# Kernel tuning notes

Hardware: AMD Instinct MI355X
Metric: run time of the kernel (lower is better)

The kernel has to match this reference:

```python
import jax, jax.numpy as jnp
import numpy as np

N_E = 1024
E_DIM = 256
BETA = 0.25
EPS = 1e-10


def setup_inputs() -> dict:
    key = jax.random.key(0)
    k1, k2 = jax.random.split(key)
    z = jax.random.normal(k1, (32, E_DIM, 32, 32), dtype=jnp.float32)
    emb = jax.random.normal(k2, (N_E, E_DIM), dtype=jnp.float32)
    return {"z": z, "emb": emb}


def reference(z, emb):
    sg = jax.lax.stop_gradient
    # (B, C, H, W) -> (B, H, W, C)
    zp = jnp.transpose(z, (0, 2, 3, 1))
    zf = zp.reshape(-1, E_DIM)  # (N, C), N = B*H*W
    # squared euclidean distances: ||z||^2 + ||e||^2 - 2 z e^T  -> (N, n_e)
    d = (jnp.sum(zf * zf, axis=1, keepdims=True)
         + jnp.sum(emb * emb, axis=1)
         - 2.0 * jnp.matmul(zf, emb.T))
    idx = jnp.argmin(d, axis=1)  # (N,)
    # one-hot @ codebook == gather (same math, no dense one-hot matmul)
    z_q1 = emb[idx].reshape(zp.shape)  # (B, H, W, C)
    # loss: note original does NOT detach z_q1 anywhere
    loss = jnp.mean((z_q1 - zp) ** 2) + BETA * jnp.mean((z_q1 - sg(zp)) ** 2)
    # straight-through (original detaches z, not z_q1)
    z_q = zp + (z_q1 - sg(zp))
    # perplexity from mean one-hot encodings = normalized histogram of indices
    counts = jnp.bincount(idx, length=N_E)
    e_mean = counts.astype(zf.dtype) / idx.shape[0]
    perplexity = jnp.exp(-jnp.sum(e_mean * jnp.log(e_mean + EPS)))
    z_q = jnp.transpose(z_q, (0, 3, 1, 2))
    z_q1_out = jnp.transpose(z_q1, (0, 3, 1, 2))
    return loss, z_q, perplexity, idx, z_q1_out
```

## Files before the change

### kernel.cpp

```cpp
#include <hip/hip_runtime.h>
#include <hip/hip_bf16.h>
#include <math.h>

#define CDIM 256
#define HW   1024
#define NVEC 32768
#define NE   1024
#define ZSIZE 8388608
#define NSPLIT 2
#define MARGIN 0.05f

#define OUT_LOSS 0
#define OUT_ZQ   1
#define OUT_PERP 8388609
#define OUT_IDX  8388610
#define OUT_ZQ1  8421378

#define WS_LOSS   0
#define WS_RCNT   64
#define WS_HIST   128
#define WS_ENORM  4224
#define WS_IDX    8448
#define WS_RLIST  139520
#define WS_S1     270592
#define WS_S2     532736
#define WS_J1     794880
#define WS_EBH    1057024
#define WS_EBL    1581312
#define WS_ZBH    2105600
#define WS_ZBL    18882816
#define WS_SCORE  WS_EBH

typedef __attribute__((ext_vector_type(8))) short short8;
typedef __attribute__((ext_vector_type(4))) float f32x4;
typedef __attribute__((ext_vector_type(8))) unsigned short ushort8v;

__device__ __forceinline__ unsigned short bf16_rne(float x) {
    union { float f; unsigned u; } v; v.f = x;
    unsigned r = v.u + 0x7FFFu + ((v.u >> 16) & 1u);
    return (unsigned short)(r >> 16);
}
__device__ __forceinline__ float bf16_to_f(unsigned short h) {
    union { unsigned u; float f; } v; v.u = ((unsigned)h) << 16;
    return v.f;
}
__device__ __forceinline__ void lds_barrier() {
    asm volatile("s_waitcnt lgkmcnt(0)\n\ts_barrier" ::: "memory");
}

__global__ __launch_bounds__(256) void vq_prep(
    const float* __restrict__ z, const float* __restrict__ emb,
    unsigned short* __restrict__ zbh, unsigned short* __restrict__ zbl,
    unsigned short* __restrict__ ebh, unsigned short* __restrict__ ebl,
    float* __restrict__ enorm)
{
    const int tid = threadIdx.x, w = tid >> 6, L = tid & 63;
    if (blockIdx.x < 512) {
        __shared__ unsigned short th[64 * 264];
        __shared__ unsigned short tl[64 * 264];
        const int b = blockIdx.x >> 4, hw0 = (blockIdx.x & 15) << 6;
        const float* zp = z + (size_t)b * (CDIM * HW) + hw0;
        for (int i = 0; i < 16; ++i) {
            int k = (i * 4 + w) * 4;
            float f0 = zp[(size_t)(k + 0) * HW + L];
            float f1 = zp[(size_t)(k + 1) * HW + L];
            float f2 = zp[(size_t)(k + 2) * HW + L];
            float f3 = zp[(size_t)(k + 3) * HW + L];
            ushort4 hi = { bf16_rne(f0), bf16_rne(f1), bf16_rne(f2), bf16_rne(f3) };
            ushort4 lo = { bf16_rne(f0 - bf16_to_f(hi.x)), bf16_rne(f1 - bf16_to_f(hi.y)),
                           bf16_rne(f2 - bf16_to_f(hi.z)), bf16_rne(f3 - bf16_to_f(hi.w)) };
            *(ushort4*)&th[L * 264 + k] = hi;
            *(ushort4*)&tl[L * 264 + k] = lo;
        }
        __syncthreads();
#pragma unroll
        for (int it = 0; it < 8; ++it) {
            int row = it * 8 + (tid >> 5);
            int kc = (tid & 31) * 8;
            size_t o = (size_t)(b * 1024 + hw0 + row) * CDIM + kc;
            *(ushort8v*)(zbh + o) = *(ushort8v*)&th[row * 264 + kc];
            *(ushort8v*)(zbl + o) = *(ushort8v*)&tl[row * 264 + kc];
        }
    } else {
        const int cb = (int)(blockIdx.x - 512) * 64;
        for (int p = 0; p < 16; ++p) {
            int code = cb + p * 4 + w;
            float4 v = *(const float4*)(emb + (size_t)code * CDIM + L * 4);
            float s = v.x * v.x + v.y * v.y + v.z * v.z + v.w * v.w;
            for (int off = 32; off; off >>= 1) s += __shfl_down(s, off, 64);
            if (L == 0) enorm[code] = s;
            ushort4 hi = { bf16_rne(v.x), bf16_rne(v.y), bf16_rne(v.z), bf16_rne(v.w) };
            ushort4 lo = { bf16_rne(v.x - bf16_to_f(hi.x)), bf16_rne(v.y - bf16_to_f(hi.y)),
                           bf16_rne(v.z - bf16_to_f(hi.z)), bf16_rne(v.w - bf16_to_f(hi.w)) };
            *(ushort4*)(ebh + (size_t)code * CDIM + L * 4) = hi;
            *(ushort4*)(ebl + (size_t)code * CDIM + L * 4) = lo;
        }
    }
}

__global__ __launch_bounds__(256, 2) void vq_mfma3(
    const unsigned short* __restrict__ zbh, const unsigned short* __restrict__ zbl,
    const unsigned short* __restrict__ ebh, const unsigned short* __restrict__ ebl,
    const float* __restrict__ enorm,
    float* __restrict__ s1_ws, float* __restrict__ s2_ws, int* __restrict__ j1_ws)
{
    __shared__ short albuf[32768];
    __shared__ short bbuf[8192];

    const int tid = threadIdx.x, w = tid >> 6, L = tid & 63;
    const int l15 = L & 15, q = L >> 4;
    const int r16 = tid & 15, ch = (tid >> 4) & 3;
    const int mtile = blockIdx.x & 255, js = blockIdx.x >> 8;
    const int n0 = mtile << 7;
    const int jsbase = js << 9;

#pragma unroll
    for (int ro = 0; ro < 16; ++ro) {
        const int seg = ro * 4 + w;
        const int sw2 = seg >> 4, smf = (seg >> 3) & 1, skk = seg & 7;
        short8 v = *(const short8*)(zbl + (size_t)(n0 + sw2 * 32 + smf * 16 + r16) * CDIM + skk * 32 + ch * 8);
        *(short8*)(albuf + seg * 512 + L * 8) = v;
    }
    short8 AH[2][8];
#pragma unroll
    for (int mf = 0; mf < 2; ++mf)
#pragma unroll
        for (int kk = 0; kk < 8; ++kk)
            AH[mf][kk] = *(const short8*)(zbh + (size_t)(n0 + w * 32 + mf * 16 + l15) * CDIM + kk * 32 + q * 8);
    __syncthreads();

    float s1[2][4], s2[2][4]; int j1[2][4];
#pragma unroll
    for (int mf = 0; mf < 2; ++mf)
#pragma unroll
        for (int r = 0; r < 4; ++r) { s1[mf][r] = -3.4e38f; s2[mf][r] = -3.4e38f; j1[mf][r] = 0; }

    for (int j0i = 0; j0i < 4; ++j0i) {
        const int j0 = jsbase + j0i * 128;
        f32x4 acc[2][8] = {};
        short8 st[4];
#pragma unroll
        for (int ro = 0; ro < 4; ++ro) {
            const unsigned short* src = (ro >= 2) ? ebl : ebh;
            const int jf = (ro & 1) * 4 + w;
            st[ro] = *(const short8*)(src + (size_t)(j0 + jf * 16 + r16) * CDIM + ch * 8);
        }
#pragma unroll
        for (int kk = 0; kk < 8; ++kk) {
            lds_barrier();
#pragma unroll
            for (int ro = 0; ro < 4; ++ro)
                *(short8*)(bbuf + (ro * 4 + w) * 512 + L * 8) = st[ro];
            if (kk < 7) {
                const int k0n = (kk + 1) * 32;
#pragma unroll
                for (int ro = 0; ro < 4; ++ro) {
                    const unsigned short* src = (ro >= 2) ? ebl : ebh;
                    const int jf = (ro & 1) * 4 + w;
                    st[ro] = *(const short8*)(src + (size_t)(j0 + jf * 16 + r16) * CDIM + k0n + ch * 8);
                }
            }
            lds_barrier();
            short8 AL0 = *(const short8*)(albuf + (w * 16 + kk) * 512 + L * 8);
            short8 AL1 = *(const short8*)(albuf + (w * 16 + 8 + kk) * 512 + L * 8);
#pragma unroll
            for (int jf = 0; jf < 8; ++jf) {
                short8 Bh = *(const short8*)(bbuf + jf * 512 + L * 8);
                short8 Bl = *(const short8*)(bbuf + (8 + jf) * 512 + L * 8);
                acc[0][jf] = __builtin_amdgcn_mfma_f32_16x16x32_bf16(AH[0][kk], Bh, acc[0][jf], 0, 0, 0);
                acc[1][jf] = __builtin_amdgcn_mfma_f32_16x16x32_bf16(AH[1][kk], Bh, acc[1][jf], 0, 0, 0);
                acc[0][jf] = __builtin_amdgcn_mfma_f32_16x16x32_bf16(AH[0][kk], Bl, acc[0][jf], 0, 0, 0);
                acc[1][jf] = __builtin_amdgcn_mfma_f32_16x16x32_bf16(AH[1][kk], Bl, acc[1][jf], 0, 0, 0);
                acc[0][jf] = __builtin_amdgcn_mfma_f32_16x16x32_bf16(AL0, Bh, acc[0][jf], 0, 0, 0);
                acc[1][jf] = __builtin_amdgcn_mfma_f32_16x16x32_bf16(AL1, Bh, acc[1][jf], 0, 0, 0);
            }
        }
#pragma unroll
        for (int jf = 0; jf < 8; ++jf) {
            const int j = j0 + jf * 16 + l15;
            const float hn = 0.5f * enorm[j];
#pragma unroll
            for (int mf = 0; mf < 2; ++mf)
#pragma unroll
                for (int r = 0; r < 4; ++r) {
                    float s = acc[mf][jf][r] - hn;
                    if (s > s1[mf][r]) { s2[mf][r] = s1[mf][r]; s1[mf][r] = s; j1[mf][r] = j; }
                    else if (s > s2[mf][r]) s2[mf][r] = s;
                }
        }
    }

#pragma unroll
    for (int mf = 0; mf < 2; ++mf)
#pragma unroll
        for (int r = 0; r < 4; ++r) {
            float a1 = s1[mf][r], a2 = s2[mf][r]; int aj = j1[mf][r];
            for (int m = 1; m < 16; m <<= 1) {
                float o1 = __shfl_xor(a1, m, 64);
                float o2 = __shfl_xor(a2, m, 64);
                int   oj = __shfl_xor(aj, m, 64);
                if (o1 > a1 || (o1 == a1 && oj < aj)) { a2 = fmaxf(a1, o2); a1 = o1; aj = oj; }
                else a2 = fmaxf(a2, o1);
            }
            if (l15 == 0) {
                int o = js * NVEC + n0 + w * 32 + mf * 16 + q * 4 + r;
                s1_ws[o] = a1; s2_ws[o] = a2; j1_ws[o] = aj;
            }
        }
}

__global__ __launch_bounds__(256) void vq_merge(
    const float* __restrict__ s1_ws, const float* __restrict__ s2_ws,
    const int* __restrict__ j1_ws, int* __restrict__ idx_ws,
    float* __restrict__ idx_out, int* __restrict__ hist,
    int* __restrict__ rcnt, int* __restrict__ rlist,
    unsigned long long* __restrict__ score)
{
    int n = blockIdx.x * 256 + threadIdx.x;
    score[n] = 0ull;
    float b1 = -3.4e38f, b2 = -3.4e38f; int bj = 0;
#pragma unroll
    for (int s = 0; s < NSPLIT; ++s) {
        float a1 = s1_ws[s * NVEC + n], a2 = s2_ws[s * NVEC + n];
        int aj = j1_ws[s * NVEC + n];
        if (a1 > b1 || (a1 == b1 && aj < bj)) { b2 = fmaxf(b1, a2); b1 = a1; bj = aj; }
        else b2 = fmaxf(b2, a1);
    }
    idx_ws[n] = bj;
    if (b1 - b2 < MARGIN) {
        int p = atomicAdd(rcnt, 1); rlist[p] = n;
    } else {
        idx_out[n] = (float)bj;
        atomicAdd(&hist[bj], 1);
    }
}

__global__ __launch_bounds__(256) void vq_rescue(
    const float* __restrict__ z, const float* __restrict__ emb,
    const float* __restrict__ enorm, const int* __restrict__ rcnt,
    const int* __restrict__ rlist, unsigned long long* __restrict__ score)
{
    __shared__ __align__(16) float zrow[256];
    __shared__ float en_s[64];
    __shared__ float rs[4];
    __shared__ int   rj[4];
    const int tid = threadIdx.x;
    const int wv = tid >> 6, L = tid & 63;
    const int chunk = blockIdx.x & 15;
    const int jwave = chunk * 64 + wv * 16;
    const int jodd = L >> 5;
    const int rstride = gridDim.x >> 4;
    const int count = *rcnt;

    for (int it = blockIdx.x >> 4; it < count; it += rstride) {
        __syncthreads();
        const int n = rlist[it];
        zrow[tid] = z[(size_t)(n >> 10) * (CDIM * HW) + (size_t)tid * HW + (n & 1023)];
        if (tid < 64) en_s[tid] = enorm[chunk * 64 + tid];
        __syncthreads();
        const float4 zv = *(const float4*)&zrow[L * 4];

        float b1 = -3.4e38f; int bj = 0x7fffffff;
#pragma unroll
        for (int jo = 0; jo < 16; jo += 2) {
            const int jA = jwave + jo;
            const float4 eA = *(const float4*)(emb + (size_t)jA * CDIM + L * 4);
            const float4 eB = *(const float4*)(emb + (size_t)(jA + 1) * CDIM + L * 4);
            float pA = fmaf(zv.x, eA.x, fmaf(zv.y, eA.y, fmaf(zv.z, eA.z, zv.w * eA.w)));
            float pB = fmaf(zv.x, eB.x, fmaf(zv.y, eB.y, fmaf(zv.z, eB.z, zv.w * eB.w)));
            float tA = pA + __shfl_xor(pA, 32, 64);
            float tB = pB + __shfl_xor(pB, 32, 64);
            float u = (L < 32) ? tA : tB;
            u += __shfl_xor(u, 16, 64);
            u += __shfl_xor(u, 8, 64);
            u += __shfl_xor(u, 4, 64);
            u += __shfl_xor(u, 2, 64);
            u += __shfl_xor(u, 1, 64);
            const int j = jA + jodd;
            const float s = u - 0.5f * en_s[wv * 16 + jo + jodd];
            if (s > b1) { b1 = s; bj = j; }
        }
        {
            const float o1 = __shfl_xor(b1, 32, 64);
            const int   oj = __shfl_xor(bj, 32, 64);
            if (o1 > b1 || (o1 == b1 && oj < bj)) { b1 = o1; bj = oj; }
        }
        if (L == 0) { rs[wv] = b1; rj[wv] = bj; }
        __syncthreads();
        if (tid == 0) {
            float f1 = rs[0]; int fj = rj[0];
#pragma unroll
            for (int v = 1; v < 4; ++v)
                if (rs[v] > f1 || (rs[v] == f1 && rj[v] < fj)) { f1 = rs[v]; fj = rj[v]; }
            unsigned key = __float_as_uint(f1);
            key = (key & 0x80000000u) ? ~key : (key | 0x80000000u);
            unsigned long long packed = ((unsigned long long)key << 32) | (unsigned)(~fj);
            atomicMax(&score[it], packed);
        }
    }
}

__global__ __launch_bounds__(256) void vq_rfin(
    const int* __restrict__ rcnt, const int* __restrict__ rlist,
    const unsigned long long* __restrict__ score, int* __restrict__ idx_ws,
    float* __restrict__ idx_out, int* __restrict__ hist)
{
    const int count = *rcnt;
    for (int it = blockIdx.x * 256 + threadIdx.x; it < count; it += gridDim.x * 256) {
        const unsigned long long p = score[it];
        const int fj = (int)(~(unsigned)p) & (NE - 1);
        const int n = rlist[it];
        idx_ws[n] = fj;
        idx_out[n] = (float)fj;
        atomicAdd(&hist[fj], 1);
    }
}

__global__ __launch_bounds__(256) void vq_gather(
    const float* __restrict__ z, const float* __restrict__ emb,
    const int* __restrict__ idx_ws, float* __restrict__ zq,
    float* __restrict__ zq1, double* __restrict__ loss_sum)
{
    __shared__ float es[32 * 129];
    __shared__ int ids[32];
    __shared__ float wred[4];

    const int tid = threadIdx.x, w = tid >> 6, L = tid & 63;
    const int b   = blockIdx.x >> 6;
    const int half = (blockIdx.x >> 5) & 1;
    const int hw0 = (blockIdx.x & 31) << 5;
    const int n0  = (b << 10) + hw0;
    const int c0  = half << 7;

    if (tid < 32) ids[tid] = idx_ws[n0 + tid];
    __syncthreads();

#pragma unroll
    for (int p = 0; p < 4; ++p) {
        int u = p * 256 + tid;
        int r = u >> 5, cq = (u & 31) * 4;
        float4 v = *(const float4*)(emb + (size_t)ids[r] * CDIM + c0 + cq);
        es[r * 129 + cq + 0] = v.x;
        es[r * 129 + cq + 1] = v.y;
        es[r * 129 + cq + 2] = v.z;
        es[r * 129 + cq + 3] = v.w;
    }
    __syncthreads();

    const int row = L & 31, cp = L >> 5;
    const size_t zbase = (size_t)b * (CDIM * HW) + hw0 + row;
    float ls = 0.f;
    for (int rd = 0; rd < 16; ++rd) {
        int cl = rd * 8 + w * 2 + cp;
        size_t off = zbase + (size_t)(c0 + cl) * HW;
        float zv = z[off];
        float e  = es[row * 129 + cl];
        float d  = e - zv;
        zq[off]  = zv + d;
        zq1[off] = e;
        ls += d * d;
    }

    for (int off = 32; off; off >>= 1) ls += __shfl_down(ls, off, 64);
    if (L == 0) wred[w] = ls;
    __syncthreads();
    if (tid == 0)
        atomicAdd(loss_sum, (double)(wred[0] + wred[1] + wred[2] + wred[3]));
}

__global__ __launch_bounds__(1024) void vq_final(
    const int* __restrict__ hist, const double* __restrict__ loss_sum,
    float* __restrict__ out_loss, float* __restrict__ out_perp)
{
    int tid = threadIdx.x;
    float em = (float)hist[tid] * (1.0f / 32768.0f);
    float term = em * logf(em + 1e-10f);
    for (int off = 32; off; off >>= 1) term += __shfl_down(term, off, 64);
    __shared__ float red[16];
    int lane = tid & 63, wv = tid >> 6;
    if (lane == 0) red[wv] = term;
    __syncthreads();
    if (tid == 0) {
        float s = 0.f;
        for (int i = 0; i < 16; ++i) s += red[i];
        *out_perp = expf(-s);
        *out_loss = (float)(*loss_sum * 1.25 / 8388608.0);
    }
}

extern "C" void kernel_launch(void* const* d_in, const int* in_sizes, int n_in,
                              void* d_out, int out_size, void* d_ws, size_t ws_size,
                              hipStream_t stream) {
    const float* z   = (const float*)d_in[0];
    const float* emb = (const float*)d_in[1];
    float* out = (float*)d_out;
    char*  ws  = (char*)d_ws;

    double* loss_sum    = (double*)(ws + WS_LOSS);
    int*    rcnt        = (int*)(ws + WS_RCNT);
    int*    hist        = (int*)(ws + WS_HIST);
    float*  enorm       = (float*)(ws + WS_ENORM);
    int*    idx_ws      = (int*)(ws + WS_IDX);
    int*    rlist       = (int*)(ws + WS_RLIST);
    float*  s1_ws       = (float*)(ws + WS_S1);
    float*  s2_ws       = (float*)(ws + WS_S2);
    int*    j1_ws       = (int*)(ws + WS_J1);
    unsigned short* ebh = (unsigned short*)(ws + WS_EBH);
    unsigned short* ebl = (unsigned short*)(ws + WS_EBL);
    unsigned short* zbh = (unsigned short*)(ws + WS_ZBH);
    unsigned short* zbl = (unsigned short*)(ws + WS_ZBL);
    unsigned long long* score = (unsigned long long*)(ws + WS_SCORE);

    hipMemsetAsync(d_ws, 0, 4224, stream);

    vq_prep  <<<528, 256, 0, stream>>>(z, emb, zbh, zbl, ebh, ebl, enorm);
    vq_mfma3 <<<512, 256, 0, stream>>>(zbh, zbl, ebh, ebl, enorm, s1_ws, s2_ws, j1_ws);
    vq_merge <<<128, 256, 0, stream>>>(s1_ws, s2_ws, j1_ws, idx_ws, out + OUT_IDX, hist, rcnt, rlist, score);
    vq_rescue<<<2048, 256, 0, stream>>>(z, emb, enorm, rcnt, rlist, score);
    vq_rfin  <<<8, 256, 0, stream>>>(rcnt, rlist, score, idx_ws, out + OUT_IDX, hist);
    vq_gather<<<2048, 256, 0, stream>>>(z, emb, idx_ws, out + OUT_ZQ, out + OUT_ZQ1, loss_sum);
    vq_final <<<1, 1024, 0, stream>>>(hist, loss_sum, out + OUT_LOSS, out + OUT_PERP);
}
```

Before: 238.7 us.

## Switch split-precision distance GEMM from bf16 to fp16 with double-buffered B tiles

Replaces the bf16 hi/lo split with an fp16 split. The codebook is kept only as an fp16 high part, so the low-part codebook term disappears and the per-step MFMA count drops from six to four. The B-tile staging loop is flattened across all code chunks with a double-buffered LDS tile, which removes one barrier per step and prefetches across chunk boundaries. The rescue margin is widened to absorb the larger rounding error, which may send more vectors to the exact-rescue path. fp16's narrower exponent range is also a risk for inputs with unusual scales.

```diff
diff --git a/kernel.cpp b/kernel.cpp
--- a/kernel.cpp
+++ b/kernel.cpp
@@ -8,7 +8,7 @@
 #define NE   1024
 #define ZSIZE 8388608
 #define NSPLIT 2
-#define MARGIN 0.05f
+#define MARGIN 0.075f
 
 #define OUT_LOSS 0
 #define OUT_ZQ   1
@@ -29,20 +29,19 @@
 #define WS_EBL    1581312
 #define WS_ZBH    2105600
 #define WS_ZBL    18882816
-#define WS_SCORE  WS_EBH
+#define WS_SCORE  WS_EBL
 
 typedef __attribute__((ext_vector_type(8))) short short8;
 typedef __attribute__((ext_vector_type(4))) float f32x4;
 typedef __attribute__((ext_vector_type(8))) unsigned short ushort8v;
-
-__device__ __forceinline__ unsigned short bf16_rne(float x) {
-    union { float f; unsigned u; } v; v.f = x;
-    unsigned r = v.u + 0x7FFFu + ((v.u >> 16) & 1u);
-    return (unsigned short)(r >> 16);
-}
-__device__ __forceinline__ float bf16_to_f(unsigned short h) {
-    union { unsigned u; float f; } v; v.u = ((unsigned)h) << 16;
-    return v.f;
+typedef __attribute__((ext_vector_type(8))) _Float16 half8;
+
+__device__ __forceinline__ unsigned short f16_rne(float x) {
+    _Float16 h = (_Float16)x;
+    return __builtin_bit_cast(unsigned short, h);
+}
+__device__ __forceinline__ float f16_to_f(unsigned short u) {
+    return (float)__builtin_bit_cast(_Float16, u);
 }
 __device__ __forceinline__ void lds_barrier() {
     asm volatile("s_waitcnt lgkmcnt(0)\n\ts_barrier" ::: "memory");
@@ -51,8 +50,7 @@
 __global__ __launch_bounds__(256) void vq_prep(
     const float* __restrict__ z, const float* __restrict__ emb,
     unsigned short* __restrict__ zbh, unsigned short* __restrict__ zbl,
-    unsigned short* __restrict__ ebh, unsigned short* __restrict__ ebl,
-    float* __restrict__ enorm)
+    unsigned short* __restrict__ ebh, float* __restrict__ enorm)
 {
     const int tid = threadIdx.x, w = tid >> 6, L = tid & 63;
     if (blockIdx.x < 512) {
@@ -66,9 +64,9 @@
             float f1 = zp[(size_t)(k + 1) * HW + L];
             float f2 = zp[(size_t)(k + 2) * HW + L];
             float f3 = zp[(size_t)(k + 3) * HW + L];
-            ushort4 hi = { bf16_rne(f0), bf16_rne(f1), bf16_rne(f2), bf16_rne(f3) };
-            ushort4 lo = { bf16_rne(f0 - bf16_to_f(hi.x)), bf16_rne(f1 - bf16_to_f(hi.y)),
-                           bf16_rne(f2 - bf16_to_f(hi.z)), bf16_rne(f3 - bf16_to_f(hi.w)) };
+            ushort4 hi = { f16_rne(f0), f16_rne(f1), f16_rne(f2), f16_rne(f3) };
+            ushort4 lo = { f16_rne(f0 - f16_to_f(hi.x)), f16_rne(f1 - f16_to_f(hi.y)),
+                           f16_rne(f2 - f16_to_f(hi.z)), f16_rne(f3 - f16_to_f(hi.w)) };
             *(ushort4*)&th[L * 264 + k] = hi;
             *(ushort4*)&tl[L * 264 + k] = lo;
         }
@@ -89,23 +87,20 @@
             float s = v.x * v.x + v.y * v.y + v.z * v.z + v.w * v.w;
             for (int off = 32; off; off >>= 1) s += __shfl_down(s, off, 64);
             if (L == 0) enorm[code] = s;
-            ushort4 hi = { bf16_rne(v.x), bf16_rne(v.y), bf16_rne(v.z), bf16_rne(v.w) };
-            ushort4 lo = { bf16_rne(v.x - bf16_to_f(hi.x)), bf16_rne(v.y - bf16_to_f(hi.y)),
-                           bf16_rne(v.z - bf16_to_f(hi.z)), bf16_rne(v.w - bf16_to_f(hi.w)) };
+            ushort4 hi = { f16_rne(v.x), f16_rne(v.y), f16_rne(v.z), f16_rne(v.w) };
             *(ushort4*)(ebh + (size_t)code * CDIM + L * 4) = hi;
-            *(ushort4*)(ebl + (size_t)code * CDIM + L * 4) = lo;
         }
     }
 }
 
 __global__ __launch_bounds__(256, 2) void vq_mfma3(
     const unsigned short* __restrict__ zbh, const unsigned short* __restrict__ zbl,
-    const unsigned short* __restrict__ ebh, const unsigned short* __restrict__ ebl,
+    const unsigned short* __restrict__ ebh,
     const float* __restrict__ enorm,
     float* __restrict__ s1_ws, float* __restrict__ s2_ws, int* __restrict__ j1_ws)
 {
     __shared__ short albuf[32768];
-    __shared__ short bbuf[8192];
+    __shared__ short bbuf[2][4096];
 
     const int tid = threadIdx.x, w = tid >> 6, L = tid & 63;
     const int l15 = L & 15, q = L >> 4;
@@ -121,12 +116,12 @@
         short8 v = *(const short8*)(zbl + (size_t)(n0 + sw2 * 32 + smf * 16 + r16) * CDIM + skk * 32 + ch * 8);
         *(short8*)(albuf + seg * 512 + L * 8) = v;
     }
-    short8 AH[2][8];
+    half8 AH[2][8];
 #pragma unroll
     for (int mf = 0; mf < 2; ++mf)
 #pragma unroll
         for (int kk = 0; kk < 8; ++kk)
-            AH[mf][kk] = *(const short8*)(zbh + (size_t)(n0 + w * 32 + mf * 16 + l15) * CDIM + kk * 32 + q * 8);
+            AH[mf][kk] = *(const half8*)(zbh + (size_t)(n0 + w * 32 + mf * 16 + l15) * CDIM + kk * 32 + q * 8);
     __syncthreads();
 
     float s1[2][4], s2[2][4]; int j1[2][4];
@@ -135,58 +130,69 @@
 #pragma unroll
         for (int r = 0; r < 4; ++r) { s1[mf][r] = -3.4e38f; s2[mf][r] = -3.4e38f; j1[mf][r] = 0; }
 
-    for (int j0i = 0; j0i < 4; ++j0i) {
-        const int j0 = jsbase + j0i * 128;
-        f32x4 acc[2][8] = {};
-        short8 st[4];
-#pragma unroll
-        for (int ro = 0; ro < 4; ++ro) {
-            const unsigned short* src = (ro >= 2) ? ebl : ebh;
-            const int jf = (ro & 1) * 4 + w;
-            st[ro] = *(const short8*)(src + (size_t)(j0 + jf * 16 + r16) * CDIM + ch * 8);
-        }
-#pragma unroll
-        for (int kk = 0; kk < 8; ++kk) {
-            lds_barrier();
-#pragma unroll
-            for (int ro = 0; ro < 4; ++ro)
-                *(short8*)(bbuf + (ro * 4 + w) * 512 + L * 8) = st[ro];
-            if (kk < 7) {
-                const int k0n = (kk + 1) * 32;
-#pragma unroll
-                for (int ro = 0; ro < 4; ++ro) {
-                    const unsigned short* src = (ro >= 2) ? ebl : ebh;
-                    const int jf = (ro & 1) * 4 + w;
-                    st[ro] = *(const short8*)(src + (size_t)(j0 + jf * 16 + r16) * CDIM + k0n + ch * 8);
-                }
+    short8 st[2];
+#pragma unroll
+    for (int ro = 0; ro < 2; ++ro)
+        st[ro] = *(const short8*)(ebh + (size_t)(jsbase + (ro * 4 + w) * 16 + r16) * CDIM + ch * 8);
+#pragma unroll
+    for (int ro = 0; ro < 2; ++ro)
+        *(short8*)(bbuf[0] + (ro * 4 + w) * 512 + L * 8) = st[ro];
+#pragma unroll
+    for (int ro = 0; ro < 2; ++ro)
+        st[ro] = *(const short8*)(ebh + (size_t)(jsbase + (ro * 4 + w) * 16 + r16) * CDIM + 32 + ch * 8);
+    lds_barrier();
+
+    f32x4 acc[2][8];
+#pragma unroll 8
+    for (int t = 0; t < 32; ++t) {
+        const int kk = t & 7;
+        if (kk == 0) {
+#pragma unroll
+            for (int mf = 0; mf < 2; ++mf)
+#pragma unroll
+                for (int jf = 0; jf < 8; ++jf)
+                    acc[mf][jf] = (f32x4){0.f, 0.f, 0.f, 0.f};
+        }
+        half8 AL0 = *(const half8*)(albuf + (w * 16 + kk) * 512 + L * 8);
+        half8 AL1 = *(const half8*)(albuf + (w * 16 + 8 + kk) * 512 + L * 8);
+        const short* bb = bbuf[t & 1];
+#pragma unroll
+        for (int jf = 0; jf < 8; ++jf) {
+            half8 Bh = *(const half8*)(bb + jf * 512 + L * 8);
+            acc[0][jf] = __builtin_amdgcn_mfma_f32_16x16x32_f16(AH[0][kk], Bh, acc[0][jf], 0, 0, 0);
+            acc[1][jf] = __builtin_amdgcn_mfma_f32_16x16x32_f16(AH[1][kk], Bh, acc[1][jf], 0, 0, 0);
+            acc[0][jf] = __builtin_amdgcn_mfma_f32_16x16x32_f16(AL0, Bh, acc[0][jf], 0, 0, 0);
+            acc[1][jf] = __builtin_amdgcn_mfma_f32_16x16x32_f16(AL1, Bh, acc[1][jf], 0, 0, 0);
+        }
+        if (t < 31) {
+#pragma unroll
+            for (int ro = 0; ro < 2; ++ro)
+                *(short8*)(bbuf[(t + 1) & 1] + (ro * 4 + w) * 512 + L * 8) = st[ro];
+            if (t < 30) {
+                const int t2 = t + 2;
+                const int j0n = jsbase + (t2 >> 3) * 128;
+                const int k0n = (t2 & 7) * 32;
+#pragma unroll
+                for (int ro = 0; ro < 2; ++ro)
+                    st[ro] = *(const short8*)(ebh + (size_t)(j0n + (ro * 4 + w) * 16 + r16) * CDIM + k0n + ch * 8);
             }
             lds_barrier();
-            short8 AL0 = *(const short8*)(albuf + (w * 16 + kk) * 512 + L * 8);
-            short8 AL1 = *(const short8*)(albuf + (w * 16 + 8 + kk) * 512 + L * 8);
+        }
+        if (kk == 7) {
+            const int j0 = jsbase + (t >> 3) * 128;
 #pragma unroll
             for (int jf = 0; jf < 8; ++jf) {
-                short8 Bh = *(const short8*)(bbuf + jf * 512 + L * 8);
-                short8 Bl = *(const short8*)(bbuf + (8 + jf) * 512 + L * 8);
-                acc[0][jf] = __builtin_amdgcn_mfma_f32_16x16x32_bf16(AH[0][kk], Bh, acc[0][jf], 0, 0, 0);
-                acc[1][jf] = __builtin_amdgcn_mfma_f32_16x16x32_bf16(AH[1][kk], Bh, acc[1][jf], 0, 0, 0);
-                acc[0][jf] = __builtin_amdgcn_mfma_f32_16x16x32_bf16(AH[0][kk], Bl, acc[0][jf], 0, 0, 0);
-                acc[1][jf] = __builtin_amdgcn_mfma_f32_16x16x32_bf16(AH[1][kk], Bl, acc[1][jf], 0, 0, 0);
-                acc[0][jf] = __builtin_amdgcn_mfma_f32_16x16x32_bf16(AL0, Bh, acc[0][jf], 0, 0, 0);
-                acc[1][jf] = __builtin_amdgcn_mfma_f32_16x16x32_bf16(AL1, Bh, acc[1][jf], 0, 0, 0);
+                const int j = j0 + jf * 16 + l15;
+                const float hn = 0.5f * enorm[j];
+#pragma unroll
+                for (int mf = 0; mf < 2; ++mf)
+#pragma unroll
+                    for (int r = 0; r < 4; ++r) {
+                        float s = acc[mf][jf][r] - hn;
+                        if (s > s1[mf][r]) { s2[mf][r] = s1[mf][r]; s1[mf][r] = s; j1[mf][r] = j; }
+                        else if (s > s2[mf][r]) s2[mf][r] = s;
+                    }
             }
-        }
-#pragma unroll
-        for (int jf = 0; jf < 8; ++jf) {
-            const int j = j0 + jf * 16 + l15;
-            const float hn = 0.5f * enorm[j];
-#pragma unroll
-            for (int mf = 0; mf < 2; ++mf)
-#pragma unroll
-                for (int r = 0; r < 4; ++r) {
-                    float s = acc[mf][jf][r] - hn;
-                    if (s > s1[mf][r]) { s2[mf][r] = s1[mf][r]; s1[mf][r] = s; j1[mf][r] = j; }
-                    else if (s > s2[mf][r]) s2[mf][r] = s;
-                }
         }
     }
 
@@ -406,15 +412,14 @@
     float*  s2_ws       = (float*)(ws + WS_S2);
     int*    j1_ws       = (int*)(ws + WS_J1);
     unsigned short* ebh = (unsigned short*)(ws + WS_EBH);
-    unsigned short* ebl = (unsigned short*)(ws + WS_EBL);
     unsigned short* zbh = (unsigned short*)(ws + WS_ZBH);
     unsigned short* zbl = (unsigned short*)(ws + WS_ZBL);
     unsigned long long* score = (unsigned long long*)(ws + WS_SCORE);
 
     hipMemsetAsync(d_ws, 0, 4224, stream);
 
-    vq_prep  <<<528, 256, 0, stream>>>(z, emb, zbh, zbl, ebh, ebl, enorm);
-    vq_mfma3 <<<512, 256, 0, stream>>>(zbh, zbl, ebh, ebl, enorm, s1_ws, s2_ws, j1_ws);
+    vq_prep  <<<528, 256, 0, stream>>>(z, emb, zbh, zbl, ebh, enorm);
+    vq_mfma3 <<<512, 256, 0, stream>>>(zbh, zbl, ebh, enorm, s1_ws, s2_ws, j1_ws);
     vq_merge <<<128, 256, 0, stream>>>(s1_ws, s2_ws, j1_ws, idx_ws, out + OUT_IDX, hist, rcnt, rlist, score);
     vq_rescue<<<2048, 256, 0, stream>>>(z, emb, enorm, rcnt, rlist, score);
     vq_rfin  <<<8, 256, 0, stream>>>(rcnt, rlist, score, idx_ws, out + OUT_IDX, hist);
```

Measured after the change: 230.5 us. -3.4%, faster.
